# Performance work log

Hardware: AMD Instinct MI355X
Metric: run time of the kernel (lower is better)

Reference implementation:

```python
import jax, jax.numpy as jnp
import numpy as np

N_NODES = 50000
N_EDGES = 500000
NUM_RADIAL = 6
HIDDEN = 128

def swish(v):
    return v * jax.nn.sigmoid(v)

def setup_inputs() -> dict:
    key = jax.random.key(0)
    ks = jax.random.split(key, 8)
    x = jax.random.randint(ks[0], (N_NODES,), 0, 95, dtype=jnp.int32)
    rbf = jax.random.normal(ks[1], (N_EDGES, NUM_RADIAL), dtype=jnp.float32)
    i = jax.random.randint(ks[2], (N_EDGES,), 0, N_NODES, dtype=jnp.int32)
    j = jax.random.randint(ks[3], (N_EDGES,), 0, N_NODES, dtype=jnp.int32)
    sqrt3 = np.sqrt(3.0).astype(np.float32)
    emb_weight = jax.random.uniform(ks[4], (95, HIDDEN), minval=-sqrt3, maxval=sqrt3, dtype=jnp.float32)
    w_rbf0 = jax.random.normal(ks[5], (HIDDEN, NUM_RADIAL), dtype=jnp.float32) * 0.2
    b_rbf0 = jnp.zeros((HIDDEN,), dtype=jnp.float32)
    w_lin = jax.random.normal(ks[6], (HIDDEN, 3 * HIDDEN), dtype=jnpp.float32) if False else jax.random.normal(ks[6], (HIDDEN, 3 * HIDDEN), dtype=jnp.float32) * 0.05
    b_lin = jnp.zeros((HIDDEN,), dtype=jnp.float32)
    w_rbf1 = jax.random.normal(ks[7], (HIDDEN, NUM_RADIAL), dtype=jnp.float32) * 0.4
    return {"x": x, "rbf": rbf, "i": i, "j": j, "emb_weight": emb_weight,
            "w_rbf0": w_rbf0, "b_rbf0": b_rbf0, "w_lin": w_lin, "b_lin": b_lin,
            "w_rbf1": w_rbf1}

def reference(x, rbf, i, j, emb_weight, w_rbf0, b_rbf0, w_lin, b_lin, w_rbf1):
    # node embedding lookup: [N, H]
    h = emb_weight[x]
    # rbf0 = swish(rbf @ W0^T + b0): [E, H]
    rbf0 = swish(jnp.einsum('er,hr->eh', rbf, w_rbf0) + b_rbf0)
    # gather endpoint embeddings and concat with rbf0: [E, 3H]
    cat = jnp.concatenate([h[i], h[j], rbf0], axis=-1)
    e1 = swish(jnp.einsum('ek,hk->eh', cat, w_lin) + b_lin)
    e2 = jnp.einsum('er,hr->eh', rbf, w_rbf1) * e1
    return (e1, e2)
```

## Files before the change

kernel.cpp:

```cpp
#include <hip/hip_runtime.h>

#define HIDDEN 128
#define NRAD 6
#define NEMB 95
#define PRS 132
#define WRS 132
#define SCR 132
#define NWAVES 12
#define NBLK 256

typedef short bf16x8 __attribute__((ext_vector_type(8)));
typedef float f32x4 __attribute__((ext_vector_type(4)));

__device__ __forceinline__ float fast_rcp(float x) { return __builtin_amdgcn_rcpf(x); }
__device__ __forceinline__ float swishf(float v) { return v * fast_rcp(1.0f + __expf(-v)); }
__device__ __forceinline__ short f2bf(float f) {
    union { float f; unsigned u; } c; c.f = f;
    unsigned r = (c.u + 0x7FFFu + ((c.u >> 16) & 1u)) >> 16;
    return (short)(unsigned short)r;
}
__device__ __forceinline__ float bf2f(unsigned short u) {
    union { unsigned u; float f; } c; c.u = ((unsigned)u) << 16; return c.f;
}
__device__ __forceinline__ unsigned pk(float lo, float hi) {
    return __builtin_amdgcn_perm(__float_as_uint(hi), __float_as_uint(lo), 0x07060302u);
}
__device__ __forceinline__ float xlo(unsigned u) {
    union { unsigned u; float f; } c; c.u = u << 16; return c.f;
}
__device__ __forceinline__ float xhi(unsigned u) {
    union { unsigned u; float f; } c; c.u = u & 0xffff0000u; return c.f;
}
__device__ __forceinline__ void wait_lgkm() {
    asm volatile("s_waitcnt lgkmcnt(0)" ::: "memory");
}

__global__ void precompute_kernel(const float* __restrict__ emb,
                                  const float* __restrict__ w_lin,
                                  const float* __restrict__ b_lin,
                                  unsigned* __restrict__ pPair) {
    __shared__ __align__(16) float erow[HIDDEN];
    const int a = blockIdx.x;
    const int h = threadIdx.x;
    erow[h] = emb[a * HIDDEN + h];
    __syncthreads();
    float a1 = b_lin[h];
    float a2 = 0.f;
    const float* __restrict__ w1 = w_lin + h * 384;
    const float* __restrict__ w2 = w1 + HIDDEN;
#pragma unroll 8
    for (int k = 0; k < HIDDEN; ++k) {
        a1 += erow[k] * w1[k];
        a2 += erow[k] * w2[k];
    }
    const unsigned lo = (unsigned)(unsigned short)f2bf(a1);
    const unsigned hi = ((unsigned)(unsigned short)f2bf(a2)) << 16;
    pPair[a * HIDDEN + h] = hi | lo;
}

struct RawMD {
    float2 ra, rb, rc;
    int ii, jj;
};

__device__ __forceinline__ RawMD load_raw(int tile, int l15, int n_edges,
                                          const int* __restrict__ iv,
                                          const int* __restrict__ jv,
                                          const float* __restrict__ rbf) {
    int e = tile * 16 + l15;
    int ecl = (e < n_edges) ? e : (n_edges - 1);
    RawMD m;
    const float2* rp = reinterpret_cast<const float2*>(rbf + (size_t)ecl * NRAD);
    m.ra = rp[0];
    m.rb = rp[1];
    m.rc = rp[2];
    m.ii = iv[ecl];
    m.jj = jv[ecl];
    return m;
}

__global__ __launch_bounds__(768)
void edge_mfma_kernel(const int* __restrict__ xv,
                      const float* __restrict__ rbf,
                      const int* __restrict__ iv,
                      const int* __restrict__ jv,
                      const float* __restrict__ w_rbf0,
                      const float* __restrict__ b_rbf0,
                      const float* __restrict__ w_rbf1,
                      const float* __restrict__ w_lin,
                      const unsigned* __restrict__ pPairG,
                      float* __restrict__ out_e1,
                      float* __restrict__ out_e2,
                      int n_edges, int nt16, int n_rows) {
    __shared__ unsigned pps[NEMB * PRS];
    __shared__ __align__(16) short w3s[HIDDEN * WRS];
    __shared__ __align__(16) short w1a[HIDDEN * 8];
    __shared__ __align__(16) unsigned short scratch[NWAVES][16 * SCR];

    const int tid = threadIdx.x;

    {
        const int nr = (n_rows < NEMB ? n_rows : NEMB);
        for (int s = tid; s < nr * HIDDEN; s += 768) {
            pps[(s >> 7) * PRS + (s & 127)] = pPairG[s];
        }
    }
    for (int s = tid; s < HIDDEN * 16; s += 768) {
        const int h = s >> 4, oct = s & 15;
        const float4* s4 = reinterpret_cast<const float4*>(w_lin + h * 384 + 256 + oct * 8);
        const float4 va = s4[0];
        const float4 vb = s4[1];
        bf16x8 fr;
        fr[0] = f2bf(va.x); fr[1] = f2bf(va.y);
        fr[2] = f2bf(va.z); fr[3] = f2bf(va.w);
        fr[4] = f2bf(vb.x); fr[5] = f2bf(vb.y);
        fr[6] = f2bf(vb.z); fr[7] = f2bf(vb.w);
        *reinterpret_cast<bf16x8*>(&w3s[h * WRS + oct * 8]) = fr;
    }
    if (tid < HIDDEN) {
        bf16x8 f1;
#pragma unroll
        for (int r = 0; r < NRAD; ++r) f1[r] = f2bf(w_rbf1[tid * NRAD + r]);
        f1[6] = 0; f1[7] = 0;
        *reinterpret_cast<bf16x8*>(&w1a[tid * 8]) = f1;
    }

    const int wid = tid >> 6;
    const int lane = tid & 63;
    const int l15 = lane & 15;
    const int lg = lane >> 4;

    bf16x8 aw0[8];
#pragma unroll
    for (int c = 0; c < 8; ++c) {
        bf16x8 fr = (bf16x8){0, 0, 0, 0, 0, 0, 0, 0};
        if (lg == 0) {
            const int k = c * 16 + l15;
#pragma unroll
            for (int r = 0; r < NRAD; ++r) fr[r] = f2bf(w_rbf0[k * NRAD + r]);
            fr[6] = f2bf(b_rbf0[k]);
            fr[7] = 0;
        }
        aw0[c] = fr;
    }
    __syncthreads();

    unsigned short* const scr = &scratch[wid][0];
    const int gw = blockIdx.x * NWAVES + wid;
    const int NW = NBLK * NWAVES;
    const f32x4 zero4 = (f32x4){0.f, 0.f, 0.f, 0.f};

    int t = gw;
    if (t < nt16) {
        RawMD cur = load_raw(t, l15, n_edges, iv, jv, rbf);
        for (; t < nt16; t += NW) {
            const int tn = (t + NW < nt16) ? t + NW : t;
            RawMD nxt = load_raw(tn, l15, n_edges, iv, jv, rbf);
            const int xi = xv[cur.ii];
            const int xj = xv[cur.jj];

            union { uint4 q; bf16x8 b; } rp;
            rp.q = (uint4){0u, 0u, 0u, 0u};
            if (lg == 0) {
                rp.q.x = pk(cur.ra.x, cur.ra.y);
                rp.q.y = pk(cur.rb.x, cur.rb.y);
                rp.q.z = pk(cur.rc.x, cur.rc.y);
                rp.q.w = pk(1.0f, 0.0f);
            }

#pragma unroll
            for (int c = 0; c < 8; ++c) {
                const f32x4 cb = __builtin_amdgcn_mfma_f32_16x16x32_bf16(
                    aw0[c], rp.b, zero4, 0, 0, 0);
                const uint2 wv = make_uint2(pk(swishf(cb[0]), swishf(cb[1])),
                                            pk(swishf(cb[2]), swishf(cb[3])));
                *reinterpret_cast<uint2*>(&scr[l15 * SCR + c * 16 + lg * 4]) = wv;
            }

            f32x4 acc2[8];
#pragma unroll
            for (int nt = 0; nt < 8; ++nt) {
                const bf16x8 aw = *reinterpret_cast<const bf16x8*>(
                    &w1a[(nt * 16 + l15) * 8]);
                acc2[nt] = __builtin_amdgcn_mfma_f32_16x16x32_bf16(aw, rp.b, zero4, 0, 0, 0);
            }

            wait_lgkm();

            bf16x8 bfrag[4];
#pragma unroll
            for (int ks = 0; ks < 4; ++ks)
                bfrag[ks] = *reinterpret_cast<const bf16x8*>(
                    &scr[l15 * SCR + ks * 32 + lg * 8]);

            f32x4 acc[8];
#pragma unroll
            for (int nt = 0; nt < 8; ++nt) acc[nt] = zero4;
#pragma unroll
            for (int ks = 0; ks < 4; ++ks)
#pragma unroll
                for (int nt = 0; nt < 8; ++nt) {
                    const bf16x8 wfr = *reinterpret_cast<const bf16x8*>(
                        &w3s[(nt * 16 + l15) * WRS + (ks * 4 + lg) * 8]);
                    acc[nt] = __builtin_amdgcn_mfma_f32_16x16x32_bf16(
                        wfr, bfrag[ks], acc[nt], 0, 0, 0);
                }

#pragma unroll
            for (int p = 0; p < 2; ++p) {
                if ((l15 >> 3) == p) {
                    const int so = (l15 & 7) * SCR;
#pragma unroll
                    for (int nt = 0; nt < 8; ++nt) {
                        const int ch0 = nt * 16 + lg * 4;
                        const uint4 r1 = *reinterpret_cast<const uint4*>(&pps[xi * PRS + ch0]);
                        const uint4 r2 = *reinterpret_cast<const uint4*>(&pps[xj * PRS + ch0]);
                        const unsigned rr1[4] = {r1.x, r1.y, r1.z, r1.w};
                        const unsigned rr2[4] = {r2.x, r2.y, r2.z, r2.w};
                        float e1v[4], e2v[4];
#pragma unroll
                        for (int q = 0; q < 4; ++q) {
                            const float pv = bf2f((unsigned short)(rr1[q] & 0xffff))
                                           + bf2f((unsigned short)(rr2[q] >> 16));
                            const float sm = acc[nt][q] + pv;
                            e1v[q] = swishf(sm);
                            e2v[q] = acc2[nt][q] * e1v[q];
                        }
                        *reinterpret_cast<uint2*>(&scr[so + ch0]) =
                            make_uint2(pk(e1v[0], e1v[1]), pk(e1v[2], e1v[3]));
                        *reinterpret_cast<uint2*>(&scr[(8 + (l15 & 7)) * SCR + ch0]) =
                            make_uint2(pk(e2v[0], e2v[1]), pk(e2v[2], e2v[3]));
                    }
                }
                wait_lgkm();

                const size_t base = ((size_t)t * 16 + p * 8) * HIDDEN;
#pragma unroll
                for (int arr = 0; arr < 2; ++arr) {
                    float* __restrict__ ob = arr ? out_e2 : out_e1;
#pragma unroll
                    for (int s2 = 0; s2 < 4; ++s2) {
                        const int idx = s2 * 256 + lane * 4;
                        const int e_l = idx >> 7;
                        const int ch = idx & 127;
                        const uint2 uv = *reinterpret_cast<const uint2*>(
                            &scr[(arr * 8 + e_l) * SCR + ch]);
                        if (t * 16 + p * 8 + e_l < n_edges) {
                            f32x4 v;
                            v[0] = xlo(uv.x); v[1] = xhi(uv.x);
                            v[2] = xlo(uv.y); v[3] = xhi(uv.y);
                            *reinterpret_cast<f32x4*>(ob + base + idx) = v;
                        }
                    }
                }
                wait_lgkm();
            }
            cur = nxt;
        }
    }
}

extern "C" void kernel_launch(void* const* d_in, const int* in_sizes, int n_in,
                              void* d_out, int out_size, void* d_ws, size_t ws_size,
                              hipStream_t stream) {
    const int*   xv     = (const int*)  d_in[0];
    const float* rbf    = (const float*)d_in[1];
    const int*   iv     = (const int*)  d_in[2];
    const int*   jv     = (const int*)  d_in[3];
    const float* emb    = (const float*)d_in[4];
    const float* w_rbf0 = (const float*)d_in[5];
    const float* b_rbf0 = (const float*)d_in[6];
    const float* w_lin  = (const float*)d_in[7];
    const float* b_lin  = (const float*)d_in[8];
    const float* w_rbf1 = (const float*)d_in[9];

    const int n_edges = in_sizes[2];
    const int n_emb_rows = in_sizes[4] / HIDDEN;

    unsigned* pPair = (unsigned*)d_ws;

    float* out_e1 = (float*)d_out;
    float* out_e2 = out_e1 + (size_t)n_edges * HIDDEN;

    precompute_kernel<<<n_emb_rows, HIDDEN, 0, stream>>>(emb, w_lin, b_lin, pPair);

    const int nt16 = (n_edges + 15) / 16;
    edge_mfma_kernel<<<NBLK, 768, 0, stream>>>(xv, rbf, iv, jv,
                                               w_rbf0, b_rbf0, w_rbf1, w_lin,
                                               pPair, out_e1, out_e2,
                                               n_edges, nt16, n_emb_rows);
}
```

Before: 144.1 us.

## Deepen edge-metadata prefetch to two tiles and drop half-split epilogue

Extends the software pipeline so that raw edge indices and rbf are loaded two tiles ahead and the node-type lookups xv[i]/xv[j] one tile ahead, hiding the dependent global gather latency. The epilogue no longer splits the 16-edge tile into two 8-edge halves with divergent lanes. All lanes now compute e1 for their edge, write it to scratch and store it, then reuse the scratch buffer for e2. This removes the lane-divergent branch and halves the epilogue loop count, at the cost of more live registers for the extra prefetched tile and extra LDS round-trips and waits.

```diff
diff --git a/kernel.cpp b/kernel.cpp
--- a/kernel.cpp
+++ b/kernel.cpp
@@ -153,11 +153,16 @@
     int t = gw;
     if (t < nt16) {
         RawMD cur = load_raw(t, l15, n_edges, iv, jv, rbf);
+        const int tn0 = (t + NW < nt16) ? t + NW : t;
+        RawMD nxt = load_raw(tn0, l15, n_edges, iv, jv, rbf);
+        int cxi = xv[cur.ii];
+        int cxj = xv[cur.jj];
+
         for (; t < nt16; t += NW) {
-            const int tn = (t + NW < nt16) ? t + NW : t;
-            RawMD nxt = load_raw(tn, l15, n_edges, iv, jv, rbf);
-            const int xi = xv[cur.ii];
-            const int xj = xv[cur.jj];
+            const int t2 = (t + 2 * NW < nt16) ? t + 2 * NW : t;
+            RawMD p2 = load_raw(t2, l15, n_edges, iv, jv, rbf);
+            const int gxi = xv[nxt.ii];
+            const int gxj = xv[nxt.jj];
 
             union { uint4 q; bf16x8 b; } rp;
             rp.q = (uint4){0u, 0u, 0u, 0u};
@@ -206,56 +211,68 @@
                         wfr, bfrag[ks], acc[nt], 0, 0, 0);
                 }
 
-#pragma unroll
-            for (int p = 0; p < 2; ++p) {
-                if ((l15 >> 3) == p) {
-                    const int so = (l15 & 7) * SCR;
-#pragma unroll
-                    for (int nt = 0; nt < 8; ++nt) {
-                        const int ch0 = nt * 16 + lg * 4;
-                        const uint4 r1 = *reinterpret_cast<const uint4*>(&pps[xi * PRS + ch0]);
-                        const uint4 r2 = *reinterpret_cast<const uint4*>(&pps[xj * PRS + ch0]);
-                        const unsigned rr1[4] = {r1.x, r1.y, r1.z, r1.w};
-                        const unsigned rr2[4] = {r2.x, r2.y, r2.z, r2.w};
-                        float e1v[4], e2v[4];
-#pragma unroll
-                        for (int q = 0; q < 4; ++q) {
-                            const float pv = bf2f((unsigned short)(rr1[q] & 0xffff))
-                                           + bf2f((unsigned short)(rr2[q] >> 16));
-                            const float sm = acc[nt][q] + pv;
-                            e1v[q] = swishf(sm);
-                            e2v[q] = acc2[nt][q] * e1v[q];
-                        }
-                        *reinterpret_cast<uint2*>(&scr[so + ch0]) =
-                            make_uint2(pk(e1v[0], e1v[1]), pk(e1v[2], e1v[3]));
-                        *reinterpret_cast<uint2*>(&scr[(8 + (l15 & 7)) * SCR + ch0]) =
-                            make_uint2(pk(e2v[0], e2v[1]), pk(e2v[2], e2v[3]));
-                    }
+            wait_lgkm();
+
+#pragma unroll
+            for (int nt = 0; nt < 8; ++nt) {
+                const int ch0 = nt * 16 + lg * 4;
+                const uint4 r1 = *reinterpret_cast<const uint4*>(&pps[cxi * PRS + ch0]);
+                const uint4 r2 = *reinterpret_cast<const uint4*>(&pps[cxj * PRS + ch0]);
+                const unsigned rr1[4] = {r1.x, r1.y, r1.z, r1.w};
+                const unsigned rr2[4] = {r2.x, r2.y, r2.z, r2.w};
+                float e1v[4];
+#pragma unroll
+                for (int q = 0; q < 4; ++q) {
+                    const float pv = bf2f((unsigned short)(rr1[q] & 0xffff))
+                                   + bf2f((unsigned short)(rr2[q] >> 16));
+                    const float sm = acc[nt][q] + pv;
+                    e1v[q] = swishf(sm);
+                    acc2[nt][q] *= e1v[q];
                 }
-                wait_lgkm();
-
-                const size_t base = ((size_t)t * 16 + p * 8) * HIDDEN;
-#pragma unroll
-                for (int arr = 0; arr < 2; ++arr) {
-                    float* __restrict__ ob = arr ? out_e2 : out_e1;
-#pragma unroll
-                    for (int s2 = 0; s2 < 4; ++s2) {
-                        const int idx = s2 * 256 + lane * 4;
-                        const int e_l = idx >> 7;
-                        const int ch = idx & 127;
-                        const uint2 uv = *reinterpret_cast<const uint2*>(
-                            &scr[(arr * 8 + e_l) * SCR + ch]);
-                        if (t * 16 + p * 8 + e_l < n_edges) {
-                            f32x4 v;
-                            v[0] = xlo(uv.x); v[1] = xhi(uv.x);
-                            v[2] = xlo(uv.y); v[3] = xhi(uv.y);
-                            *reinterpret_cast<f32x4*>(ob + base + idx) = v;
-                        }
-                    }
+                *reinterpret_cast<uint2*>(&scr[l15 * SCR + ch0]) =
+                    make_uint2(pk(e1v[0], e1v[1]), pk(e1v[2], e1v[3]));
+            }
+            wait_lgkm();
+
+            const size_t base = (size_t)t * 16 * HIDDEN;
+#pragma unroll
+            for (int s2 = 0; s2 < 8; ++s2) {
+                const int idx = s2 * 256 + lane * 4;
+                const int e_l = idx >> 7;
+                const int ch = idx & 127;
+                const uint2 uv = *reinterpret_cast<const uint2*>(&scr[e_l * SCR + ch]);
+                if (t * 16 + e_l < n_edges) {
+                    f32x4 v;
+                    v[0] = xlo(uv.x); v[1] = xhi(uv.x);
+                    v[2] = xlo(uv.y); v[3] = xhi(uv.y);
+                    *reinterpret_cast<f32x4*>(out_e1 + base + idx) = v;
                 }
-                wait_lgkm();
-            }
-            cur = nxt;
+            }
+            wait_lgkm();
+
+#pragma unroll
+            for (int nt = 0; nt < 8; ++nt) {
+                const int ch0 = nt * 16 + lg * 4;
+                *reinterpret_cast<uint2*>(&scr[l15 * SCR + ch0]) =
+                    make_uint2(pk(acc2[nt][0], acc2[nt][1]), pk(acc2[nt][2], acc2[nt][3]));
+            }
+            wait_lgkm();
+#pragma unroll
+            for (int s2 = 0; s2 < 8; ++s2) {
+                const int idx = s2 * 256 + lane * 4;
+                const int e_l = idx >> 7;
+                const int ch = idx & 127;
+                const uint2 uv = *reinterpret_cast<const uint2*>(&scr[e_l * SCR + ch]);
+                if (t * 16 + e_l < n_edges) {
+                    f32x4 v;
+                    v[0] = xlo(uv.x); v[1] = xhi(uv.x);
+                    v[2] = xlo(uv.y); v[3] = xhi(uv.y);
+                    *reinterpret_cast<f32x4*>(out_e2 + base + idx) = v;
+                }
+            }
+            wait_lgkm();
+
+            cur = nxt; nxt = p2; cxi = gxi; cxj = gxj;
         }
     }
 }
```

After: 158.6 us. 10.1% more time.
